# Performance work log

Hardware: AMD Instinct MI355X
Metric: run time of the kernel (lower is better)

## Reference

```python
import jax, jax.numpy as jnp
import numpy as np

B, L, D = 4, 2048, 1024
EV = 64            # event_embed_dim
EXPAND = 2
DI = EXPAND * D    # d_inner = 2048
N = 16             # d_state
K = 4              # d_conv
DT_RANK = (D + 15) // 16  # 64
EPS = 1e-5


def setup_inputs() -> dict:
    key = jax.random.key(0)
    ks = jax.random.split(key, 16)
    g = lambda k, shape, s=0.02: (jax.random.normal(k, shape, dtype=jnp.float32) * s)
    return {
        "x": jax.random.normal(ks[0], (B, L, D), dtype=jnp.float32),
        "event_emb": jax.random.normal(ks[1], (B, L, EV), dtype=jnp.float32),
        "W_in": g(ks[2], (D + EV, D)),
        "b_in": jnp.zeros((D,), jnp.float32),
        "ln_g": jnp.ones((D,), jnp.float32),
        "ln_b": jnp.zeros((D,), jnp.float32),
        "in_proj_w": g(ks[3], (D, 2 * DI)),
        "conv_w": g(ks[4], (DI, K), 0.1),
        "conv_b": jnp.zeros((DI,), jnp.float32),
        "x_proj_w": g(ks[5], (DI, DT_RANK + 2 * N)),
        "dt_proj_w": g(ks[6], (DT_RANK, DI), 0.1),
        "dt_proj_b": jnp.full((DI,), -4.6, jnp.float32),  # ~softplus^-1(0.01)
        "A_log": jnp.log(jnp.broadcast_to(jnp.arange(1, N + 1, dtype=jnp.float32), (DI, N))),
        "D_param": jnp.ones((DI,), jnp.float32),
        "out_proj_w": g(ks[7], (DI, D)),
    }


def _mamba_block(x, event_emb, W_in, b_in, ln_g, ln_b, in_proj_w, conv_w, conv_b,
                 x_proj_w, dt_proj_w, dt_proj_b, A_log, D_param, out_proj_w):
    d_conv = conv_w.shape[1]
    n_state = A_log.shape[1]
    dt_rank = dt_proj_w.shape[0]
    Lx = x.shape[1]

    aug = jnp.concatenate([x, event_emb], axis=-1) @ W_in + b_in   # [B,L,D]
    residual = aug
    mu = aug.mean(-1, keepdims=True)
    var = jnp.mean((aug - mu) ** 2, axis=-1, keepdims=True)
    h = (aug - mu) * jax.lax.rsqrt(var + EPS) * ln_g + ln_b

    xz = h @ in_proj_w                                             # [B,L,2*DI]
    xh, z = jnp.split(xz, 2, axis=-1)

    # causal depthwise conv1d (width d_conv)
    xp = jnp.pad(xh, ((0, 0), (d_conv - 1, 0), (0, 0)))
    xc = conv_b
    for k in range(d_conv):
        xc = xc + conv_w[:, k] * xp[:, k:k + Lx, :]
    xc = jax.nn.silu(xc)                                           # [B,L,DI]

    dbl = xc @ x_proj_w                                            # [B,L,dt_rank+2N]
    dt, Bm, Cm = jnp.split(dbl, [dt_rank, dt_rank + n_state], axis=-1)
    dt = jax.nn.softplus(dt @ dt_proj_w + dt_proj_b)               # [B,L,DI]
    A = -jnp.exp(A_log)                                            # [DI,N]

    def step(hst, inp):
        dt_t, B_t, C_t, u_t = inp                                  # [B,DI],[B,N],[B,N],[B,DI]
        dA = jnp.exp(dt_t[:, :, None] * A)                         # [B,DI,N]
        dBu = (dt_t * u_t)[:, :, None] * B_t[:, None, :]           # [B,DI,N]
        hst = dA * hst + dBu
        y_t = jnp.einsum('bdn,bn->bd', hst, C_t)
        return hst, y_t

    h0 = jnp.zeros((xc.shape[0], xc.shape[2], n_state), xc.dtype)
    xs = (dt.transpose(1, 0, 2), Bm.transpose(1, 0, 2),
          Cm.transpose(1, 0, 2), xc.transpose(1, 0, 2))
    _, ys = jax.lax.scan(step, h0, xs)                             # [L,B,DI]
    y = ys.transpose(1, 0, 2) + D_param * xc
    y = y * jax.nn.silu(z)
    return residual + y @ out_proj_w                               # [B,L,D]


def reference(x, event_emb, W_in, b_in, ln_g, ln_b, in_proj_w, conv_w, conv_b,
              x_proj_w, dt_proj_w, dt_proj_b, A_log, D_param, out_proj_w):
    return _mamba_block(x, event_emb, W_in, b_in, ln_g, ln_b, in_proj_w, conv_w,
                        conv_b, x_proj_w, dt_proj_w, dt_proj_b, A_log, D_param,
                        out_proj_w)
```

## Files before the change

### kernel.cpp

```cpp
#include <hip/hip_runtime.h>
#include <cstdint>
#include <cstddef>

#define DEV __device__ __forceinline__

typedef __bf16 bf16x8 __attribute__((ext_vector_type(8)));
typedef float f32x4 __attribute__((ext_vector_type(4)));

DEV unsigned short f2bf(float f) {
  unsigned u = __builtin_bit_cast(unsigned, f);
  u += 0x7fffu + ((u >> 16) & 1u);
  return (unsigned short)(u >> 16);
}
DEV float bf2f(unsigned short h) {
  return __builtin_bit_cast(float, (unsigned)h << 16);
}

struct TransJob { const float* in; unsigned short* out; int R, C, Rout, Cout, gx; };

__global__ __launch_bounds__(256)
void k_prep(const float* __restrict__ x, const float* __restrict__ ev,
            unsigned short* __restrict__ Aaug,
            const float* __restrict__ W_in, unsigned short* __restrict__ WinT,
            const float* __restrict__ ipW, unsigned short* __restrict__ ipT,
            const float* __restrict__ xpW, unsigned short* __restrict__ xpT,
            const float* __restrict__ dpW, unsigned short* __restrict__ dpT,
            const float* __restrict__ opW, unsigned short* __restrict__ opT) {
  int tid = threadIdx.x;
  int idx = blockIdx.x;
  if (idx < 16384) {
    int col4 = (idx & 1) * 256 + tid;
    if (col4 >= 288) return;
    size_t row = idx >> 1;
    float4 v = make_float4(0.f, 0.f, 0.f, 0.f);
    if (col4 < 256)      v = reinterpret_cast<const float4*>(x + row * 1024)[col4];
    else if (col4 < 272) v = reinterpret_cast<const float4*>(ev + row * 64)[col4 - 256];
    ushort4 o; o.x = f2bf(v.x); o.y = f2bf(v.y); o.z = f2bf(v.z); o.w = f2bf(v.w);
    reinterpret_cast<ushort4*>(Aaug + row * 1152)[col4] = o;
    return;
  }
  idx -= 16384;
  const float* in; unsigned short* out; int R, C, Rout, Cout, gx;
  if (idx < 1152)      { in = W_in; out = WinT; R = 1088; C = 1024; Rout = 1152; Cout = 1024; gx = 32; }
  else if ((idx -= 1152) < 4096) { in = ipW; out = ipT; R = 1024; C = 4096; Rout = 1024; Cout = 4096; gx = 128; }
  else if ((idx -= 4096) < 256)  { in = xpW; out = xpT; R = 2048; C = 96;   Rout = 2048; Cout = 128;  gx = 4;   }
  else if ((idx -= 256) < 128)   { in = dpW; out = dpT; R = 64;   C = 2048; Rout = 64;   Cout = 2048; gx = 64;  }
  else                 { idx -= 128; in = opW; out = opT; R = 2048; C = 1024; Rout = 2048; Cout = 1024; gx = 32; }
  int cx = idx % gx, ry = idx / gx;
  __shared__ float tile[32][33];
  int c0 = cx * 32, r0 = ry * 32;
  int tx = tid & 31, ty = tid >> 5;
#pragma unroll
  for (int i = 0; i < 4; ++i) {
    int r = r0 + ty + i * 8, c = c0 + tx;
    tile[ty + i * 8][tx] = (r < R && c < C) ? in[(size_t)r * C + c] : 0.f;
  }
  __syncthreads();
#pragma unroll
  for (int i = 0; i < 4; ++i) {
    int c = c0 + ty + i * 8, r = r0 + tx;
    if (c < Cout && r < Rout) out[(size_t)c * Rout + r] = f2bf(tile[tx][ty + i * 8]);
  }
}

template <int BN, int EPI>
__global__ __launch_bounds__(512, 1)
void k_gemm8(const unsigned short* __restrict__ A, const unsigned short* __restrict__ Bt,
             int N, int NT, int lda, int ldb,
             float* __restrict__ outF, unsigned short* __restrict__ outB1,
             unsigned short* __restrict__ outB2,
             const float* __restrict__ bias, const unsigned short* __restrict__ residB) {
  static_assert(BN == 128 || BN == 256, "");
  constexpr int NF = BN / 64;
  constexpr int NHF = NF / 2;
  constexpr int BLOADS = BN / 128;
  constexpr int ATILE = 256 * 64;
  constexpr int BTILE = BN * 64;
  constexpr int BUFSZ = ATILE + BTILE;
  __shared__ unsigned short lds[2 * BUFSZ];

  const int tid = threadIdx.x;
  const int lane = tid & 63, w = tid >> 6;
  const int wm = w >> 2, wn = w & 3;
  const int frow = lane & 15, fk = lane >> 4;

  const int nbx = gridDim.x;
  const int nwg = nbx * gridDim.y;
  const int orig = blockIdx.y * nbx + blockIdx.x;
  const int swz = (orig & 7) * (nwg >> 3) + (orig >> 3);
  const int brow = swz / nbx, bcol = swz % nbx;
  const size_t row0 = (size_t)brow * 256, col0 = (size_t)bcol * BN;

  f32x4 acc[8][NF];
#pragma unroll
  for (int i = 0; i < 8; ++i)
#pragma unroll
    for (int j = 0; j < NF; ++j) acc[i][j] = f32x4{0.f, 0.f, 0.f, 0.f};

  bf16x8 afr[4][2], bq0[NHF][2], bq1[NHF][2];

  const int srow = tid >> 3;
  const int g8 = ((tid & 7) ^ (srow & 7)) * 8;
  const size_t offA_h0l0 = (row0 + 0 * 128 + 0 * 64 + srow) * (size_t)lda + g8;
  const size_t offA_h0l1 = (row0 + 1 * 128 + 0 * 64 + srow) * (size_t)lda + g8;
  const size_t offA_h1l0 = (row0 + 0 * 128 + 1 * 64 + srow) * (size_t)lda + g8;
  const size_t offA_h1l1 = (row0 + 1 * 128 + 1 * 64 + srow) * (size_t)lda + g8;
  const size_t offB_h0l0 = (col0 + 0 * (BN / 2) + 0 * 64 + srow) * (size_t)ldb + g8;
  const size_t offB_h1l0 = (col0 + 1 * (BN / 2) + 0 * 64 + srow) * (size_t)ldb + g8;
  const size_t offB_h0l1 = (BLOADS == 2) ? ((col0 + 0 * (BN / 2) + 1 * 64 + srow) * (size_t)ldb + g8) : 0;
  const size_t offB_h1l1 = (BLOADS == 2) ? ((col0 + 1 * (BN / 2) + 1 * 64 + srow) * (size_t)ldb + g8) : 0;

  char* ldsb = reinterpret_cast<char*>(lds);
  const int fr7 = frow & 7;
  const int slot0 = (fk ^ fr7) * 16;
  const int slot1 = ((4 + fk) ^ fr7) * 16;
  const int abase0 = (wm * 128 + frow) * 128 + slot0;
  const int abase1 = (wm * 128 + frow) * 128 + slot1;
  const int bbase0 = (wn * (BN / 4) + frow) * 128 + slot0 + ATILE * 2;
  const int bbase1 = (wn * (BN / 4) + frow) * 128 + slot1 + ATILE * 2;

  auto stageA = [&](int p, int tau, int half) {
    const size_t kadd = (size_t)tau * 64;
    const unsigned short* s0 = A + (half ? offA_h1l0 : offA_h0l0) + kadd;
    const unsigned short* s1 = A + (half ? offA_h1l1 : offA_h0l1) + kadd;
    unsigned short* dst = lds + p * BUFSZ + half * 4096 + w * 512;
    __builtin_amdgcn_global_load_lds(s0, dst, 16, 0, 0);
    __builtin_amdgcn_global_load_lds(s1, dst + 8192, 16, 0, 0);
  };
  auto stageB = [&](int p, int tau, int half) {
    const size_t kadd = (size_t)tau * 64;
    unsigned short* dst = lds + p * BUFSZ + ATILE + half * (BTILE / 2) + w * 512;
    const unsigned short* s0 = Bt + (half ? offB_h1l0 : offB_h0l0) + kadd;
    __builtin_amdgcn_global_load_lds(s0, dst, 16, 0, 0);
    if constexpr (BLOADS == 2) {
      const unsigned short* s1 = Bt + (half ? offB_h1l1 : offB_h0l1) + kadd;
      __builtin_amdgcn_global_load_lds(s1, dst + 4096, 16, 0, 0);
    }
  };
  auto ldA = [&](int p, int mh) {
    const int pb = p * (BUFSZ * 2);
#pragma unroll
    for (int mi = 0; mi < 4; ++mi) {
      const int off = pb + (mh * 64 + mi * 16) * 128;
      afr[mi][0] = *reinterpret_cast<const bf16x8*>(ldsb + abase0 + off);
      afr[mi][1] = *reinterpret_cast<const bf16x8*>(ldsb + abase1 + off);
    }
  };
  auto ldB = [&](int p, int nh, bf16x8 (&bq)[NHF][2]) {
    const int pb = p * (BUFSZ * 2);
#pragma unroll
    for (int ni = 0; ni < NHF; ++ni) {
      const int off = pb + (nh * (BN / 8) + ni * 16) * 128;
      bq[ni][0] = *reinterpret_cast<const bf16x8*>(ldsb + bbase0 + off);
      bq[ni][1] = *reinterpret_cast<const bf16x8*>(ldsb + bbase1 + off);
    }
  };

#define MMAQ(MH, NH, BQ)                                                          \
  do {                                                                            \
    _Pragma("unroll") for (int mi = 0; mi < 4; ++mi)                              \
        _Pragma("unroll") for (int ni = 0; ni < NHF; ++ni)                        \
            _Pragma("unroll") for (int kb = 0; kb < 2; ++kb)                      \
                acc[(MH)*4 + mi][(NH)*NHF + ni] =                                 \
                    __builtin_amdgcn_mfma_f32_16x16x32_bf16(                      \
                        afr[mi][kb], BQ[ni][kb], acc[(MH)*4 + mi][(NH)*NHF + ni], \
                        0, 0, 0);                                                 \
  } while (0)

#define PRIO1 __builtin_amdgcn_s_setprio(1)
#define PRIO0 __builtin_amdgcn_s_setprio(0)
#define BARC  __builtin_amdgcn_s_barrier()
#define SBAR  __builtin_amdgcn_sched_barrier(0)
#define VMCNT_WAIT                                                     \
  do {                                                                 \
    if constexpr (BN == 256)                                           \
      asm volatile("s_waitcnt vmcnt(6)" ::: "memory");                 \
    else                                                               \
      asm volatile("s_waitcnt vmcnt(4)" ::: "memory");                 \
  } while (0)

  stageA(0, 0, 0); stageB(0, 0, 0); stageB(0, 0, 1); stageA(0, 0, 1);
  SBAR;
  stageA(1, 1, 0); stageB(1, 1, 0); stageB(1, 1, 1);
  VMCNT_WAIT;
  BARC; SBAR;

  const int niter = NT >> 1;
  for (int it = 0; it < niter; ++it) {
    int t = 2 * it;
    int t1s = t + 1;
    int t2s = (t + 2 < NT) ? t + 2 : NT - 1;
    int t3s = (t + 3 < NT) ? t + 3 : NT - 1;
    ldA(0, 0); ldB(0, 0, bq0); ldB(0, 1, bq1);
    stageA(1, t1s, 1);
    BARC; PRIO1; MMAQ(0, 0, bq0); MMAQ(0, 1, bq1); PRIO0; BARC;
    ldA(0, 1);
    stageA(0, t2s, 0); stageB(0, t2s, 0); stageB(0, t2s, 1);
    VMCNT_WAIT;
    BARC; PRIO1; MMAQ(1, 1, bq1); MMAQ(1, 0, bq0); PRIO0; BARC;
    ldA(1, 0); ldB(1, 0, bq0); ldB(1, 1, bq1);
    stageA(0, t2s, 1);
    BARC; PRIO1; MMAQ(0, 0, bq0); MMAQ(0, 1, bq1); PRIO0; BARC;
    ldA(1, 1);
    stageA(1, t3s, 0); stageB(1, t3s, 0); stageB(1, t3s, 1);
    VMCNT_WAIT;
    BARC; PRIO1; MMAQ(1, 1, bq1); MMAQ(1, 0, bq0); PRIO0; BARC;
  }

#pragma unroll
  for (int q = 0; q < 8; ++q) {
#pragma unroll
    for (int j = 0; j < NF; ++j) {
#pragma unroll
      for (int r = 0; r < 4; ++r) {
        size_t row = row0 + wm * 128 + q * 16 + fk * 4 + r;
        size_t col = col0 + wn * (BN / 4) + j * 16 + frow;
        float v = acc[q][j][r];
        if constexpr (EPI == 0) {
          outB1[row * N + col] = f2bf(v + bias[col]);
        } else if constexpr (EPI == 1) {
          int hn = N >> 1;
          if ((int)col < hn) outB1[row * hn + col] = f2bf(v);
          else               outB2[row * hn + (col - hn)] = f2bf(v);
        } else {
          outF[row * N + col] = bf2f(residB[row * N + col]) + v;
        }
      }
    }
  }
#undef MMAQ
#undef PRIO1
#undef PRIO0
#undef BARC
#undef SBAR
#undef VMCNT_WAIT
}

template <int EPI>
__global__ __launch_bounds__(256)
void k_gemm(const unsigned short* __restrict__ A, const unsigned short* __restrict__ Bt,
            int N, int K, int lda, int ldb,
            unsigned short* __restrict__ outB1, const float* __restrict__ bias,
            float* __restrict__ outF) {
  __shared__ alignas(16) unsigned short sA[128 * 64];
  __shared__ alignas(16) unsigned short sB[128 * 64];
  int tid = threadIdx.x;
  int lane = tid & 63, w = tid >> 6;
  int nbx = gridDim.x;
  int nwg = nbx * gridDim.y;
  int orig = blockIdx.y * nbx + blockIdx.x;
  int swz = (orig & 7) * (nwg >> 3) + (orig >> 3);
  int brow = swz / nbx, bcol = swz % nbx;
  size_t row0 = (size_t)brow * 128, col0 = (size_t)bcol * 128;
  int ks = 0;
  if constexpr (EPI == 6) { ks = bcol; col0 = 0; }
  const size_t kbase = (size_t)ks * 1024;

  int lrow_s = tid >> 3;
  int g_s = tid & 7;
  int wrow = (w >> 1) * 64, wcol = (w & 1) * 64;
  int frow = lane & 15, fk = lane >> 4;
  f32x4 acc[4][4] = {};

  for (int kt = 0; kt < K; kt += 64) {
    __syncthreads();
#pragma unroll
    for (int r = 0; r < 4; ++r) {
      int lr = r * 32 + lrow_s;
      int gs = g_s ^ (lr & 7);
      const unsigned short* srcA = A + (size_t)(row0 + lr) * lda + kbase + kt + gs * 8;
      const unsigned short* srcB = Bt + (size_t)(col0 + lr) * ldb + kbase + kt + gs * 8;
      unsigned short* dstA = sA + (r * 32 + w * 8) * 64;
      unsigned short* dstB = sB + (r * 32 + w * 8) * 64;
      __builtin_amdgcn_global_load_lds(srcA, dstA, 16, 0, 0);
      __builtin_amdgcn_global_load_lds(srcB, dstB, 16, 0, 0);
    }
    __syncthreads();
#pragma unroll
    for (int kw = 0; kw < 2; ++kw) {
      bf16x8 af[4], bfr[4];
      int gk = kw * 4 + fk;
#pragma unroll
      for (int mi = 0; mi < 4; ++mi) {
        int rr = wrow + mi * 16 + frow;
        af[mi] = *reinterpret_cast<const bf16x8*>(sA + rr * 64 + ((gk ^ (rr & 7)) * 8));
      }
#pragma unroll
      for (int ni = 0; ni < 4; ++ni) {
        int rr = wcol + ni * 16 + frow;
        bfr[ni] = *reinterpret_cast<const bf16x8*>(sB + rr * 64 + ((gk ^ (rr & 7)) * 8));
      }
#pragma unroll
      for (int mi = 0; mi < 4; ++mi)
#pragma unroll
        for (int ni = 0; ni < 4; ++ni)
          acc[mi][ni] = __builtin_amdgcn_mfma_f32_16x16x32_bf16(af[mi], bfr[ni], acc[mi][ni], 0, 0, 0);
    }
  }

#pragma unroll
  for (int mi = 0; mi < 4; ++mi) {
#pragma unroll
    for (int ni = 0; ni < 4; ++ni) {
#pragma unroll
      for (int r = 0; r < 4; ++r) {
        size_t row = row0 + wrow + mi * 16 + fk * 4 + r;
        size_t col = col0 + wcol + ni * 16 + frow;
        float v = acc[mi][ni][r];
        if constexpr (EPI == 6) {
          outF[(size_t)ks * (8192ull * 128) + row * 128 + col] = v;
        } else {
          float xx = v + bias[col];
          float sp = (xx > 15.f) ? xx : __logf(1.f + __expf(xx));
          outB1[row * N + col] = f2bf(sp);
        }
      }
    }
  }
}

__global__ __launch_bounds__(256)
void k_comb(const float* __restrict__ P, unsigned short* __restrict__ dbl) {
  size_t i4 = (size_t)blockIdx.x * 256 + threadIdx.x;
  float4 a = reinterpret_cast<const float4*>(P)[i4];
  float4 b = reinterpret_cast<const float4*>(P + 8192ull * 128)[i4];
  ushort4 o;
  o.x = f2bf(a.x + b.x); o.y = f2bf(a.y + b.y);
  o.z = f2bf(a.z + b.z); o.w = f2bf(a.w + b.w);
  reinterpret_cast<ushort4*>(dbl)[i4] = o;
}

__global__ __launch_bounds__(256)
void k_ln(const unsigned short* __restrict__ aug, const float* __restrict__ gam,
          const float* __restrict__ bet, unsigned short* __restrict__ h) {
  int tid = threadIdx.x;
  size_t row = blockIdx.x;
  ushort4 raw = reinterpret_cast<const ushort4*>(aug + row * 1024)[tid];
  float v0 = bf2f(raw.x), v1 = bf2f(raw.y), v2 = bf2f(raw.z), v3 = bf2f(raw.w);
  float s = v0 + v1 + v2 + v3;
  float ss = v0 * v0 + v1 * v1 + v2 * v2 + v3 * v3;
#pragma unroll
  for (int m = 32; m >= 1; m >>= 1) {
    s += __shfl_xor(s, m, 64);
    ss += __shfl_xor(ss, m, 64);
  }
  __shared__ float rb[8];
  if ((tid & 63) == 0) { rb[tid >> 6] = s; rb[4 + (tid >> 6)] = ss; }
  __syncthreads();
  float ts = rb[0] + rb[1] + rb[2] + rb[3];
  float tss = rb[4] + rb[5] + rb[6] + rb[7];
  float mu = ts * (1.f / 1024.f);
  float var = tss * (1.f / 1024.f) - mu * mu;
  float rs = rsqrtf(var + 1e-5f);
  float4 gv = reinterpret_cast<const float4*>(gam)[tid];
  float4 bv = reinterpret_cast<const float4*>(bet)[tid];
  ushort4 o;
  o.x = f2bf((v0 - mu) * rs * gv.x + bv.x);
  o.y = f2bf((v1 - mu) * rs * gv.y + bv.y);
  o.z = f2bf((v2 - mu) * rs * gv.z + bv.z);
  o.w = f2bf((v3 - mu) * rs * gv.w + bv.w);
  reinterpret_cast<ushort4*>(h + row * 1024)[tid] = o;
}

__global__ __launch_bounds__(256)
void k_conv(const unsigned short* __restrict__ xh, const float* __restrict__ cw,
            const float* __restrict__ cb, unsigned short* __restrict__ xc) {
  size_t row = blockIdx.x;
  int t = (int)(row & 2047);
  size_t rowb = row - t;
  int d = threadIdx.x * 8;
  float acc[8];
  {
    float4 c0 = *reinterpret_cast<const float4*>(cb + d);
    float4 c1 = *reinterpret_cast<const float4*>(cb + d + 4);
    acc[0] = c0.x; acc[1] = c0.y; acc[2] = c0.z; acc[3] = c0.w;
    acc[4] = c1.x; acc[5] = c1.y; acc[6] = c1.z; acc[7] = c1.w;
  }
  float wv[8][4];
#pragma unroll
  for (int j = 0; j < 8; ++j) {
    float4 cj = *reinterpret_cast<const float4*>(cw + (size_t)(d + j) * 4);
    wv[j][0] = cj.x; wv[j][1] = cj.y; wv[j][2] = cj.z; wv[j][3] = cj.w;
  }
#pragma unroll
  for (int k = 0; k < 4; ++k) {
    int tt = t - 3 + k;
    if (tt >= 0) {
      ushort4 va = reinterpret_cast<const ushort4*>(xh + (rowb + tt) * 2048 + d)[0];
      ushort4 vb = reinterpret_cast<const ushort4*>(xh + (rowb + tt) * 2048 + d)[1];
      unsigned short e[8] = {va.x, va.y, va.z, va.w, vb.x, vb.y, vb.z, vb.w};
#pragma unroll
      for (int j = 0; j < 8; ++j) acc[j] += wv[j][k] * bf2f(e[j]);
    }
  }
  ushort4 o0, o1;
#pragma unroll
  for (int j = 0; j < 8; ++j) {
    float sg = 1.f / (1.f + __expf(-acc[j]));
    unsigned short r = f2bf(acc[j] * sg);
    if (j < 4) (&o0.x)[j] = r; else (&o1.x)[j - 4] = r;
  }
  reinterpret_cast<ushort4*>(xc + row * 2048 + d)[0] = o0;
  reinterpret_cast<ushort4*>(xc + row * 2048 + d)[1] = o1;
}

template <bool FINAL>
__global__ __launch_bounds__(256)
void k_scan(const unsigned short* __restrict__ dt, const unsigned short* __restrict__ xc,
            const unsigned short* __restrict__ dbl, const float* __restrict__ A_log,
            float* __restrict__ S, float* __restrict__ SD,
            const float* __restrict__ Hin, const float* __restrict__ Dp,
            const unsigned short* __restrict__ z, unsigned short* __restrict__ yg) {
  int d = blockIdx.x * 256 + threadIdx.x;
  int b = blockIdx.y, c = blockIdx.z;
  int t0 = c * 32;
  size_t hoff = (((size_t)c * 4 + b) * 2048 + d) * 16;
  float An[16], h[16];
  bool fast = true;
#pragma unroll
  for (int n = 0; n < 16; ++n) {
    An[n] = -__expf(A_log[((size_t)d << 4) + n]);
    fast = fast && (__builtin_fabsf(An[n] + (float)(n + 1)) < 1e-4f);
    h[n] = FINAL ? Hin[hoff + n] : 0.f;
  }
  float Dv = FINAL ? Dp[d] : 0.f;
  float dts = 0.f;
  __shared__ float sBC[32][32];
  if (threadIdx.x < 128) {
    int s = threadIdx.x >> 2, j8 = (threadIdx.x & 3) * 8;
    size_t rowg = (size_t)b * 2048 + t0 + s;
    uint4 raw = *reinterpret_cast<const uint4*>(dbl + rowg * 128 + 64 + j8);
    unsigned rr4[4] = {raw.x, raw.y, raw.z, raw.w};
#pragma unroll
    for (int q = 0; q < 4; ++q) {
      sBC[s][j8 + 2 * q]     = bf2f((unsigned short)(rr4[q] & 0xffffu));
      sBC[s][j8 + 2 * q + 1] = bf2f((unsigned short)(rr4[q] >> 16));
    }
  }
  __syncthreads();

  if (fast) {
    for (int si = 0; si < 32; ++si) {
      size_t rr = ((size_t)b * 2048 + t0 + si) * 2048 + d;
      float dtv = bf2f(dt[rr]);
      float uv = bf2f(xc[rr]);
      float dtu = dtv * uv;
      float y = 0.f;
      if constexpr (!FINAL) dts += dtv;
      float e1 = __expf(-dtv);
      float e2 = e1 * e1;
      float e3 = e2 * e1, e4 = e2 * e2;
      float e8 = e4 * e4, e12 = e8 * e4;
      float base[4] = {e1, e2, e3, e4};
      float mul[4] = {1.f, e4, e8, e12};
#pragma unroll
      for (int n = 0; n < 16; ++n) {
        float a = base[n & 3] * mul[n >> 2];
        h[n] = a * h[n] + dtu * sBC[si][n];
        if constexpr (FINAL) y += h[n] * sBC[si][16 + n];
      }
      if constexpr (FINAL) {
        float zv = bf2f(z[rr]);
        float sig = 1.f / (1.f + __expf(-zv));
        yg[rr] = f2bf((y + Dv * uv) * (zv * sig));
      }
    }
  } else {
    for (int si = 0; si < 32; ++si) {
      size_t rr = ((size_t)b * 2048 + t0 + si) * 2048 + d;
      float dtv = bf2f(dt[rr]);
      float uv = bf2f(xc[rr]);
      float dtu = dtv * uv;
      float y = 0.f;
      if constexpr (!FINAL) dts += dtv;
#pragma unroll
      for (int n = 0; n < 16; ++n) {
        float a = __expf(dtv * An[n]);
        h[n] = a * h[n] + dtu * sBC[si][n];
        if constexpr (FINAL) y += h[n] * sBC[si][16 + n];
      }
      if constexpr (FINAL) {
        float zv = bf2f(z[rr]);
        float sig = 1.f / (1.f + __expf(-zv));
        yg[rr] = f2bf((y + Dv * uv) * (zv * sig));
      }
    }
  }
  if constexpr (!FINAL) {
#pragma unroll
    for (int n = 0; n < 16; ++n) S[hoff + n] = h[n];
    SD[((size_t)c * 4 + b) * 2048 + d] = dts;
  }
}

__global__ __launch_bounds__(256)
void k_scanB(float* __restrict__ S, const float* __restrict__ SD,
             const float* __restrict__ A_log) {
  int id = blockIdx.x * 256 + threadIdx.x;
  int n = id & 15, d = (id >> 4) & 2047, b = id >> 15;
  float An = -__expf(A_log[((size_t)d << 4) + n]);
  float h = 0.f;
  for (int c = 0; c < 64; ++c) {
    size_t sdo = ((size_t)c * 4 + b) * 2048 + d;
    size_t o = sdo * 16 + n;
    float s = S[o];
    float p = __expf(An * SD[sdo]);
    S[o] = h;
    h = s + p * h;
  }
}

extern "C" void kernel_launch(void* const* d_in, const int* in_sizes, int n_in,
                              void* d_out, int out_size, void* d_ws, size_t ws_size,
                              hipStream_t stream) {
  const float* x       = (const float*)d_in[0];
  const float* ev      = (const float*)d_in[1];
  const float* W_in    = (const float*)d_in[2];
  const float* b_in    = (const float*)d_in[3];
  const float* ln_g    = (const float*)d_in[4];
  const float* ln_b    = (const float*)d_in[5];
  const float* in_proj = (const float*)d_in[6];
  const float* conv_w  = (const float*)d_in[7];
  const float* conv_b  = (const float*)d_in[8];
  const float* x_proj  = (const float*)d_in[9];
  const float* dt_proj = (const float*)d_in[10];
  const float* dt_b    = (const float*)d_in[11];
  const float* A_log   = (const float*)d_in[12];
  const float* D_par   = (const float*)d_in[13];
  const float* out_w   = (const float*)d_in[14];
  float* out = (float*)d_out;

  char* ws = (char*)d_ws;
  size_t off = 0;
  auto alloc = [&](size_t bytes) {
    char* p = ws + off;
    off = (off + bytes + 255) & ~(size_t)255;
    return p;
  };
  unsigned short* augb  = (unsigned short*)alloc(8192ull * 1024 * 2);
  unsigned short* dtfb  = (unsigned short*)alloc(8192ull * 2048 * 2);
  unsigned short* Aaug  = (unsigned short*)alloc(8192ull * 1152 * 2);
  unsigned short* WinT  = (unsigned short*)alloc(1024ull * 1152 * 2);
  unsigned short* ipT   = (unsigned short*)alloc(4096ull * 1024 * 2);
  unsigned short* xpT   = (unsigned short*)alloc(128ull * 2048 * 2);
  unsigned short* dpT   = (unsigned short*)alloc(2048ull * 64 * 2);
  unsigned short* opT   = (unsigned short*)alloc(1024ull * 2048 * 2);
  unsigned short* xh    = (unsigned short*)alloc(8192ull * 2048 * 2);
  unsigned short* zb    = (unsigned short*)alloc(8192ull * 2048 * 2);
  unsigned short* xcb   = (unsigned short*)alloc(8192ull * 2048 * 2);
  unsigned short* dbl   = (unsigned short*)alloc(8192ull * 128 * 2);
  float* Pd = (float*)alloc(2ull * 8192 * 128 * 4);
  float* Sb = (float*)alloc(64ull * 4 * 2048 * 16 * 4);
  float* SD = (float*)alloc(64ull * 4 * 2048 * 4);
  unsigned short* hb = Aaug;
  unsigned short* yg = xh;

  k_prep<<<dim3(24064), 256, 0, stream>>>(x, ev, Aaug, W_in, WinT, in_proj, ipT,
                                          x_proj, xpT, dt_proj, dpT, out_w, opT);

  k_gemm8<128, 0><<<dim3(8, 32), 512, 0, stream>>>(Aaug, WinT, 1024, 18, 1152, 1152,
                                                   nullptr, augb, nullptr, b_in, nullptr);
  k_ln<<<dim3(8192), 256, 0, stream>>>(augb, ln_g, ln_b, hb);
  k_gemm8<256, 1><<<dim3(16, 32), 512, 0, stream>>>(hb, ipT, 4096, 16, 1024, 1024,
                                                    nullptr, xh, zb, nullptr, nullptr);
  k_conv<<<dim3(8192), 256, 0, stream>>>(xh, conv_w, conv_b, xcb);
  k_gemm<6><<<dim3(2, 64), 256, 0, stream>>>(xcb, xpT, 128, 1024, 2048, 2048,
                                             nullptr, nullptr, Pd);
  k_comb<<<dim3(1024), 256, 0, stream>>>(Pd, dbl);
  k_gemm<3><<<dim3(16, 64), 256, 0, stream>>>(dbl, dpT, 2048, 64, 128, 64,
                                              dtfb, dt_b, nullptr);
  k_scan<false><<<dim3(8, 4, 64), 256, 0, stream>>>(dtfb, xcb, dbl, A_log, Sb, SD,
                                                    nullptr, nullptr, nullptr, nullptr);
  k_scanB<<<dim3(512), 256, 0, stream>>>(Sb, SD, A_log);
  k_scan<true><<<dim3(8, 4, 64), 256, 0, stream>>>(dtfb, xcb, dbl, A_log, nullptr, nullptr,
                                                   Sb, D_par, zb, yg);
  k_gemm8<128, 4><<<dim3(8, 32), 512, 0, stream>>>(yg, opT, 1024, 32, 2048, 2048,
                                                   out, nullptr, nullptr, nullptr, augb);
}
```

Before: 378.4 us.

## Split-K the input and output projection GEMMs with BN=256 tiles and combine kernels

The W_in and out_proj GEMMs now use 256x256 tiles with a two-way split along K (blockIdx.z), writing bf16 partial sums to scratch buffers. Separate combine kernels add the partials: one fused with bias and LayerNorm, one with the residual add. The K dimension of the augmented input is padded to 1280 so each split is a whole number of 64-wide steps. The aim is larger tiles with better reuse while keeping 256 blocks in flight. In exchange it adds partial-sum traffic, an extra launch, and bf16 rounding of the partials.

```diff
diff --git a/kernel.cpp b/kernel.cpp
--- a/kernel.cpp
+++ b/kernel.cpp
@@ -15,8 +15,6 @@
 DEV float bf2f(unsigned short h) {
   return __builtin_bit_cast(float, (unsigned)h << 16);
 }
-
-struct TransJob { const float* in; unsigned short* out; int R, C, Rout, Cout, gx; };
 
 __global__ __launch_bounds__(256)
 void k_prep(const float* __restrict__ x, const float* __restrict__ ev,
@@ -30,19 +28,19 @@
   int idx = blockIdx.x;
   if (idx < 16384) {
     int col4 = (idx & 1) * 256 + tid;
-    if (col4 >= 288) return;
+    if (col4 >= 320) return;
     size_t row = idx >> 1;
     float4 v = make_float4(0.f, 0.f, 0.f, 0.f);
     if (col4 < 256)      v = reinterpret_cast<const float4*>(x + row * 1024)[col4];
     else if (col4 < 272) v = reinterpret_cast<const float4*>(ev + row * 64)[col4 - 256];
     ushort4 o; o.x = f2bf(v.x); o.y = f2bf(v.y); o.z = f2bf(v.z); o.w = f2bf(v.w);
-    reinterpret_cast<ushort4*>(Aaug + row * 1152)[col4] = o;
+    reinterpret_cast<ushort4*>(Aaug + row * 1280)[col4] = o;
     return;
   }
   idx -= 16384;
   const float* in; unsigned short* out; int R, C, Rout, Cout, gx;
-  if (idx < 1152)      { in = W_in; out = WinT; R = 1088; C = 1024; Rout = 1152; Cout = 1024; gx = 32; }
-  else if ((idx -= 1152) < 4096) { in = ipW; out = ipT; R = 1024; C = 4096; Rout = 1024; Cout = 4096; gx = 128; }
+  if (idx < 1280)      { in = W_in; out = WinT; R = 1088; C = 1024; Rout = 1280; Cout = 1024; gx = 32; }
+  else if ((idx -= 1280) < 4096) { in = ipW; out = ipT; R = 1024; C = 4096; Rout = 1024; Cout = 4096; gx = 128; }
   else if ((idx -= 4096) < 256)  { in = xpW; out = xpT; R = 2048; C = 96;   Rout = 2048; Cout = 128;  gx = 4;   }
   else if ((idx -= 256) < 128)   { in = dpW; out = dpT; R = 64;   C = 2048; Rout = 64;   Cout = 2048; gx = 64;  }
   else                 { idx -= 128; in = opW; out = opT; R = 2048; C = 1024; Rout = 2048; Cout = 1024; gx = 32; }
@@ -63,21 +61,22 @@
   }
 }
 
-template <int BN, int EPI>
+template <int EPI>
 __global__ __launch_bounds__(512, 1)
 void k_gemm8(const unsigned short* __restrict__ A, const unsigned short* __restrict__ Bt,
-             int N, int NT, int lda, int ldb,
-             float* __restrict__ outF, unsigned short* __restrict__ outB1,
-             unsigned short* __restrict__ outB2,
-             const float* __restrict__ bias, const unsigned short* __restrict__ residB) {
-  static_assert(BN == 128 || BN == 256, "");
+             int N, int NT, int lda, int ldb, int KS,
+             unsigned short* __restrict__ outB1, unsigned short* __restrict__ outB2,
+             size_t pstride) {
+  constexpr int BN = 256;
   constexpr int NF = BN / 64;
   constexpr int NHF = NF / 2;
-  constexpr int BLOADS = BN / 128;
   constexpr int ATILE = 256 * 64;
   constexpr int BTILE = BN * 64;
   constexpr int BUFSZ = ATILE + BTILE;
   __shared__ unsigned short lds[2 * BUFSZ];
+
+  A += (size_t)blockIdx.z * KS;
+  Bt += (size_t)blockIdx.z * KS;
 
   const int tid = threadIdx.x;
   const int lane = tid & 63, w = tid >> 6;
@@ -105,10 +104,10 @@
   const size_t offA_h0l1 = (row0 + 1 * 128 + 0 * 64 + srow) * (size_t)lda + g8;
   const size_t offA_h1l0 = (row0 + 0 * 128 + 1 * 64 + srow) * (size_t)lda + g8;
   const size_t offA_h1l1 = (row0 + 1 * 128 + 1 * 64 + srow) * (size_t)lda + g8;
-  const size_t offB_h0l0 = (col0 + 0 * (BN / 2) + 0 * 64 + srow) * (size_t)ldb + g8;
-  const size_t offB_h1l0 = (col0 + 1 * (BN / 2) + 0 * 64 + srow) * (size_t)ldb + g8;
-  const size_t offB_h0l1 = (BLOADS == 2) ? ((col0 + 0 * (BN / 2) + 1 * 64 + srow) * (size_t)ldb + g8) : 0;
-  const size_t offB_h1l1 = (BLOADS == 2) ? ((col0 + 1 * (BN / 2) + 1 * 64 + srow) * (size_t)ldb + g8) : 0;
+  const size_t offB_h0l0 = (col0 + 0 * 128 + 0 * 64 + srow) * (size_t)ldb + g8;
+  const size_t offB_h0l1 = (col0 + 0 * 128 + 1 * 64 + srow) * (size_t)ldb + g8;
+  const size_t offB_h1l0 = (col0 + 1 * 128 + 0 * 64 + srow) * (size_t)ldb + g8;
+  const size_t offB_h1l1 = (col0 + 1 * 128 + 1 * 64 + srow) * (size_t)ldb + g8;
 
   char* ldsb = reinterpret_cast<char*>(lds);
   const int fr7 = frow & 7;
@@ -131,11 +130,9 @@
     const size_t kadd = (size_t)tau * 64;
     unsigned short* dst = lds + p * BUFSZ + ATILE + half * (BTILE / 2) + w * 512;
     const unsigned short* s0 = Bt + (half ? offB_h1l0 : offB_h0l0) + kadd;
+    const unsigned short* s1 = Bt + (half ? offB_h1l1 : offB_h0l1) + kadd;
     __builtin_amdgcn_global_load_lds(s0, dst, 16, 0, 0);
-    if constexpr (BLOADS == 2) {
-      const unsigned short* s1 = Bt + (half ? offB_h1l1 : offB_h0l1) + kadd;
-      __builtin_amdgcn_global_load_lds(s1, dst + 4096, 16, 0, 0);
-    }
+    __builtin_amdgcn_global_load_lds(s1, dst + 4096, 16, 0, 0);
   };
   auto ldA = [&](int p, int mh) {
     const int pb = p * (BUFSZ * 2);
@@ -171,13 +168,7 @@
 #define PRIO0 __builtin_amdgcn_s_setprio(0)
 #define BARC  __builtin_amdgcn_s_barrier()
 #define SBAR  __builtin_amdgcn_sched_barrier(0)
-#define VMCNT_WAIT                                                     \
-  do {                                                                 \
-    if constexpr (BN == 256)                                           \
-      asm volatile("s_waitcnt vmcnt(6)" ::: "memory");                 \
-    else                                                               \
-      asm volatile("s_waitcnt vmcnt(4)" ::: "memory");                 \
-  } while (0)
+#define VMCNT_WAIT asm volatile("s_waitcnt vmcnt(6)" ::: "memory")
 
   stageA(0, 0, 0); stageB(0, 0, 0); stageB(0, 0, 1); stageA(0, 0, 1);
   SBAR;
@@ -207,6 +198,7 @@
     BARC; PRIO1; MMAQ(1, 1, bq1); MMAQ(1, 0, bq0); PRIO0; BARC;
   }
 
+  unsigned short* pb = (EPI == 5) ? (outB1 + (size_t)blockIdx.z * pstride) : outB1;
 #pragma unroll
   for (int q = 0; q < 8; ++q) {
 #pragma unroll
@@ -216,14 +208,12 @@
         size_t row = row0 + wm * 128 + q * 16 + fk * 4 + r;
         size_t col = col0 + wn * (BN / 4) + j * 16 + frow;
         float v = acc[q][j][r];
-        if constexpr (EPI == 0) {
-          outB1[row * N + col] = f2bf(v + bias[col]);
-        } else if constexpr (EPI == 1) {
+        if constexpr (EPI == 1) {
           int hn = N >> 1;
           if ((int)col < hn) outB1[row * hn + col] = f2bf(v);
           else               outB2[row * hn + (col - hn)] = f2bf(v);
         } else {
-          outF[row * N + col] = bf2f(residB[row * N + col]) + v;
+          pb[row * N + col] = f2bf(v);
         }
       }
     }
@@ -331,12 +321,20 @@
 }
 
 __global__ __launch_bounds__(256)
-void k_ln(const unsigned short* __restrict__ aug, const float* __restrict__ gam,
-          const float* __restrict__ bet, unsigned short* __restrict__ h) {
+void k_lnc(const unsigned short* __restrict__ P, const float* __restrict__ bias,
+           const float* __restrict__ gam, const float* __restrict__ bet,
+           unsigned short* __restrict__ augb, unsigned short* __restrict__ h) {
   int tid = threadIdx.x;
   size_t row = blockIdx.x;
-  ushort4 raw = reinterpret_cast<const ushort4*>(aug + row * 1024)[tid];
-  float v0 = bf2f(raw.x), v1 = bf2f(raw.y), v2 = bf2f(raw.z), v3 = bf2f(raw.w);
+  ushort4 a0 = reinterpret_cast<const ushort4*>(P + row * 1024)[tid];
+  ushort4 a1 = reinterpret_cast<const ushort4*>(P + 8192ull * 1024 + row * 1024)[tid];
+  float4 bb = reinterpret_cast<const float4*>(bias)[tid];
+  float v0 = bf2f(a0.x) + bf2f(a1.x) + bb.x;
+  float v1 = bf2f(a0.y) + bf2f(a1.y) + bb.y;
+  float v2 = bf2f(a0.z) + bf2f(a1.z) + bb.z;
+  float v3 = bf2f(a0.w) + bf2f(a1.w) + bb.w;
+  ushort4 ro; ro.x = f2bf(v0); ro.y = f2bf(v1); ro.z = f2bf(v2); ro.w = f2bf(v3);
+  reinterpret_cast<ushort4*>(augb + row * 1024)[tid] = ro;
   float s = v0 + v1 + v2 + v3;
   float ss = v0 * v0 + v1 * v1 + v2 * v2 + v3 * v3;
 #pragma unroll
@@ -360,6 +358,21 @@
   o.z = f2bf((v2 - mu) * rs * gv.z + bv.z);
   o.w = f2bf((v3 - mu) * rs * gv.w + bv.w);
   reinterpret_cast<ushort4*>(h + row * 1024)[tid] = o;
+}
+
+__global__ __launch_bounds__(256)
+void k_outc(const unsigned short* __restrict__ P, const unsigned short* __restrict__ residB,
+            float* __restrict__ out) {
+  size_t i4 = (size_t)blockIdx.x * 256 + threadIdx.x;
+  ushort4 p0 = reinterpret_cast<const ushort4*>(P)[i4];
+  ushort4 p1 = reinterpret_cast<const ushort4*>(P + 8192ull * 1024)[i4];
+  ushort4 rr = reinterpret_cast<const ushort4*>(residB)[i4];
+  float4 o;
+  o.x = bf2f(rr.x) + bf2f(p0.x) + bf2f(p1.x);
+  o.y = bf2f(rr.y) + bf2f(p0.y) + bf2f(p1.y);
+  o.z = bf2f(rr.z) + bf2f(p0.z) + bf2f(p1.z);
+  o.w = bf2f(rr.w) + bf2f(p0.w) + bf2f(p1.w);
+  reinterpret_cast<float4*>(out)[i4] = o;
 }
 
 __global__ __launch_bounds__(256)
@@ -539,8 +552,8 @@
   };
   unsigned short* augb  = (unsigned short*)alloc(8192ull * 1024 * 2);
   unsigned short* dtfb  = (unsigned short*)alloc(8192ull * 2048 * 2);
-  unsigned short* Aaug  = (unsigned short*)alloc(8192ull * 1152 * 2);
-  unsigned short* WinT  = (unsigned short*)alloc(1024ull * 1152 * 2);
+  unsigned short* Aaug  = (unsigned short*)alloc(8192ull * 1280 * 2);
+  unsigned short* WinT  = (unsigned short*)alloc(1024ull * 1280 * 2);
   unsigned short* ipT   = (unsigned short*)alloc(4096ull * 1024 * 2);
   unsigned short* xpT   = (unsigned short*)alloc(128ull * 2048 * 2);
   unsigned short* dpT   = (unsigned short*)alloc(2048ull * 64 * 2);
@@ -552,17 +565,19 @@
   float* Pd = (float*)alloc(2ull * 8192 * 128 * 4);
   float* Sb = (float*)alloc(64ull * 4 * 2048 * 16 * 4);
   float* SD = (float*)alloc(64ull * 4 * 2048 * 4);
-  unsigned short* hb = Aaug;
-  unsigned short* yg = xh;
-
-  k_prep<<<dim3(24064), 256, 0, stream>>>(x, ev, Aaug, W_in, WinT, in_proj, ipT,
+  unsigned short* hb   = Aaug;
+  unsigned short* Paug = xh;
+  unsigned short* Pout = zb;
+  unsigned short* yg   = xh;
+
+  k_prep<<<dim3(24192), 256, 0, stream>>>(x, ev, Aaug, W_in, WinT, in_proj, ipT,
                                           x_proj, xpT, dt_proj, dpT, out_w, opT);
 
-  k_gemm8<128, 0><<<dim3(8, 32), 512, 0, stream>>>(Aaug, WinT, 1024, 18, 1152, 1152,
-                                                   nullptr, augb, nullptr, b_in, nullptr);
-  k_ln<<<dim3(8192), 256, 0, stream>>>(augb, ln_g, ln_b, hb);
-  k_gemm8<256, 1><<<dim3(16, 32), 512, 0, stream>>>(hb, ipT, 4096, 16, 1024, 1024,
-                                                    nullptr, xh, zb, nullptr, nullptr);
+  k_gemm8<5><<<dim3(4, 32, 2), 512, 0, stream>>>(Aaug, WinT, 1024, 10, 1280, 1280, 640,
+                                                 Paug, nullptr, 8192ull * 1024);
+  k_lnc<<<dim3(8192), 256, 0, stream>>>(Paug, b_in, ln_g, ln_b, augb, hb);
+  k_gemm8<1><<<dim3(16, 32, 1), 512, 0, stream>>>(hb, ipT, 4096, 16, 1024, 1024, 0,
+                                                  xh, zb, 0);
   k_conv<<<dim3(8192), 256, 0, stream>>>(xh, conv_w, conv_b, xcb);
   k_gemm<6><<<dim3(2, 64), 256, 0, stream>>>(xcb, xpT, 128, 1024, 2048, 2048,
                                              nullptr, nullptr, Pd);
@@ -574,6 +589,7 @@
   k_scanB<<<dim3(512), 256, 0, stream>>>(Sb, SD, A_log);
   k_scan<true><<<dim3(8, 4, 64), 256, 0, stream>>>(dtfb, xcb, dbl, A_log, nullptr, nullptr,
                                                    Sb, D_par, zb, yg);
-  k_gemm8<128, 4><<<dim3(8, 32), 512, 0, stream>>>(yg, opT, 1024, 32, 2048, 2048,
-                                                   out, nullptr, nullptr, nullptr, augb);
-}
+  k_gemm8<5><<<dim3(4, 32, 2), 512, 0, stream>>>(yg, opT, 1024, 16, 2048, 2048, 1024,
+                                                 Pout, nullptr, 8192ull * 1024);
+  k_outc<<<dim3(8192), 256, 0, stream>>>(Pout, augb, out);
+}
```

New measurement: 392.0 us. +3.6%, slower.
